# Optimization experiments

Hardware: AMD Instinct MI355X
Metric: run time of the kernel (lower is better)

The kernel has to match this reference:

```python
import jax, jax.numpy as jnp
import numpy as np

B, D_IN, T, H, OUT = 128, 128, 1024, 512, 2


def setup_inputs() -> dict:
    key = jax.random.key(0)
    ks = jax.random.split(key, 12)
    s = 1.0 / np.sqrt(H)  # torch LSTM/Linear init scale
    u = lambda k, shape: jax.random.uniform(k, shape, jnp.float32, -s, s)
    return {
        "x": jax.random.normal(ks[0], (B, D_IN, T), jnp.float32),
        # layer 0 (input_dim -> H), gate order i,f,g,o stacked along 4H
        "Wih0": u(ks[1], (4 * H, D_IN)),
        "Whh0": u(ks[2], (4 * H, H)),
        "bih0": u(ks[3], (4 * H,)),
        "bhh0": u(ks[4], (4 * H,)),
        # layer 1 (H -> H)
        "Wih1": u(ks[5], (4 * H, H)),
        "Whh1": u(ks[6], (4 * H, H)),
        "bih1": u(ks[7], (4 * H,)),
        "bhh1": u(ks[8], (4 * H,)),
        # linear head
        "fcW": u(ks[9], (OUT, H)),
        "fcb": u(ks[10], (OUT,)),
    }


def _lstm_layer(x_btd, Wih, Whh, bih, bhh):
    """One unidirectional LSTM layer. x_btd: (B,T,D). Returns (hs_bth, h_last)."""
    h_dim = Whh.shape[1]
    b = x_btd.shape[0]
    # precompute input contribution for all timesteps: (T, B, 4H)
    xg = jnp.einsum("btd,gd->tbg", x_btd, Wih) + (bih + bhh)

    def step(carry, xg_t):
        h, c = carry
        gates = xg_t + h @ Whh.T  # (B, 4H)
        i, f, g, o = jnp.split(gates, 4, axis=-1)
        i = jax.nn.sigmoid(i)
        f = jax.nn.sigmoid(f)
        g = jnp.tanh(g)
        o = jax.nn.sigmoid(o)
        c = f * c + i * g
        h = o * jnp.tanh(c)
        return (h, c), h

    h0 = jnp.zeros((b, h_dim), x_btd.dtype)
    c0 = jnp.zeros((b, h_dim), x_btd.dtype)
    (h_last, _), hs = jax.lax.scan(step, (h0, c0), xg)
    return jnp.transpose(hs, (1, 0, 2)), h_last  # (B,T,H), (B,H)


def reference(x, Wih0, Whh0, bih0, bhh0, Wih1, Whh1, bih1, bhh1, fcW, fcb):
    x_btd = jnp.transpose(x, (0, 2, 1))  # (B, T, D_IN), mirrors x.transpose(1,2)
    hs0, _ = _lstm_layer(x_btd, Wih0, Whh0, bih0, bhh0)
    _, h_last = _lstm_layer(hs0, Wih1, Whh1, bih1, bhh1)
    return h_last @ fcW.T + fcb  # fc(hidden[-1]) -> (B, OUT)
```

## Files before the change

kernel.cpp:

```cpp
#include <hip/hip_runtime.h>
#include <hip/hip_fp16.h>


typedef _Float16 half8 __attribute__((ext_vector_type(8)));
typedef float f32x4 __attribute__((ext_vector_type(4)));
typedef unsigned long long u64;
typedef u64 u64x2 __attribute__((ext_vector_type(2)));

#define MFMA16(a, b, c) __builtin_amdgcn_mfma_f32_16x16x32_f16((a), (b), (c), 0, 0, 0)

#define WS_H0_OFF (64 << 10)
#define WS_H1_OFF (576 << 10)
#define WS_XTW_OFF (832 << 10)
#define SYNC_CLAIM 1024
#define SYNC_MODE 1040
#define SYNC_ARRIVE 1056
#define SYNC_FLAG0 1280
#define SYNC_FLAG1 2304

__device__ __forceinline__ float sigf(float x) {
  return __builtin_amdgcn_rcpf(1.f + exp2f(-1.44269504f * x));
}
__device__ __forceinline__ float tanhf_(float x) {
  return 1.f - 2.f * __builtin_amdgcn_rcpf(1.f + exp2f(2.88539008f * x));
}
__device__ __forceinline__ unsigned short f2h(float x) {
  _Float16 h = (_Float16)x;
  unsigned short b;
  __builtin_memcpy(&b, &h, 2);
  return b;
}
__device__ __forceinline__ u64 lda(const u64* p) {
  return __hip_atomic_load(p, __ATOMIC_RELAXED, __HIP_MEMORY_SCOPE_AGENT);
}

__device__ __forceinline__ void cvt_split(const f32x4& a, const f32x4& b,
                                          half8& hi, half8& lo) {
#pragma unroll
  for (int i = 0; i < 4; ++i) {
    float w0 = a[i], w1 = b[i];
    _Float16 h0 = (_Float16)w0, h1 = (_Float16)w1;
    hi[i] = h0;
    hi[i + 4] = h1;
    lo[i] = (_Float16)((w0 - (float)h0) * 2048.0f);
    lo[i + 4] = (_Float16)((w1 - (float)h1) * 2048.0f);
  }
}
__device__ __forceinline__ half8 hscale(half8 v) {
  half8 r;
#pragma unroll
  for (int i = 0; i < 8; ++i) r[i] = v[i] * (_Float16)4.8828125e-4f;
  return r;
}

__global__ void __launch_bounds__(256) prep_kernel(const float* __restrict__ x,
                                                   _Float16* __restrict__ xTw,
                                                   unsigned* __restrict__ sync,
                                                   float* __restrict__ out) {
  const int bid = blockIdx.x;
  const int c = bid >> 4, b16 = bid & 15;
  const int tid = threadIdx.x;
  if (bid == 0) {
#pragma unroll
    for (int i = 0; i < 16; ++i) sync[i * 256 + tid] = 0;
    out[tid] = 0.f;
  }
  const int d = tid & 127, th = tid >> 7;
  const float* src = x + ((size_t)(c * 16 + b16) * 128 + d) * 1024 + th * 16;
  _Float16* dst = xTw + ((size_t)c * 32 + th * 16) * (16 * 128) + b16 * 128 + d;
#pragma unroll
  for (int i = 0; i < 16; ++i) dst[(size_t)i * (16 * 128)] = (_Float16)src[i];
}

__global__ void __launch_bounds__(256, 2) lstm_scan(
    const float* __restrict__ Whh0, const float* __restrict__ bih0,
    const float* __restrict__ bhh0, const float* __restrict__ Wih1,
    const float* __restrict__ Whh1, const float* __restrict__ bih1,
    const float* __restrict__ bhh1, const float* __restrict__ fcW,
    const float* __restrict__ fcb, const float* __restrict__ Wih0,
    const float* __restrict__ x, unsigned* __restrict__ sync,
    unsigned short* __restrict__ exch, _Float16* __restrict__ xTw,
    float* __restrict__ out) {
  __shared__ __align__(16) _Float16 hbuf[2][16][4][16][8];
  __shared__ unsigned s_bcast[2];

  const int tid = threadIdx.x;
  const int wave = tid >> 6;
  const int lane = tid & 63;
  const int q = lane >> 4;
  const int bb = lane & 15;

  unsigned xcc;
  asm("s_getreg_b32 %0, hwreg(HW_REG_XCC_ID)" : "=s"(xcc));
  xcc &= 7;
  unsigned* claim = sync + SYNC_CLAIM;
  unsigned* modew = sync + SYNC_MODE;
  unsigned* arrive = sync + SYNC_ARRIVE;
  if (tid == 0) {
    unsigned idx = __hip_atomic_fetch_add(claim + xcc, 1u, __ATOMIC_RELAXED,
                                          __HIP_MEMORY_SCOPE_AGENT);
    unsigned ord = __hip_atomic_fetch_add(arrive, 1u + (idx >> 31),
                                          __ATOMIC_RELAXED,
                                          __HIP_MEMORY_SCOPE_AGENT);
    if (ord == 511u) {
      unsigned ok = 1;
#pragma unroll
      for (int i = 0; i < 8; ++i)
        ok &= (__hip_atomic_load(claim + i, __ATOMIC_RELAXED,
                                 __HIP_MEMORY_SCOPE_AGENT) == 64u);
      __hip_atomic_store(modew, ok ? 2u : 1u, __ATOMIC_RELAXED,
                         __HIP_MEMORY_SCOPE_AGENT);
    }
    unsigned mv = 0;
    int guard = 0;
    for (;;) {
      mv = __hip_atomic_load(modew, __ATOMIC_RELAXED, __HIP_MEMORY_SCOPE_AGENT);
      if (mv != 0u) break;
      if (++guard > (1 << 18)) { mv = 1u; break; }
    }
    s_bcast[0] = mv;
    s_bcast[1] = idx;
  }
  __syncthreads();
  const bool loc = (s_bcast[0] == 2u);
  const unsigned idx = s_bcast[1];
  bool roleL1;
  int c, wg;
  if (loc) {
    c = (int)xcc;
    roleL1 = idx >= 32u;
    wg = roleL1 ? (int)idx - 32 : (int)idx;
  } else {
    const int b = blockIdx.x;
    roleL1 = b >= 256;
    const int b2 = roleL1 ? b - 256 : b;
    c = b2 >> 5;
    wg = b2 & 31;
  }

  const int wcl = wg * 4 + wave;
  const int chbase = wcl * 4;
  const int m = lane & 15;
  const int arow = (m & 3) * 512 + chbase + (m >> 2);
  unsigned short* xtw16 = (unsigned short*)xTw;
  unsigned short* exch1 = exch + ((512 << 10) >> 1);
  const int ch = chbase + q;
  const int hoff = (((ch >> 5) * 4 + ((ch >> 3) & 3)) * 16) * 8 + (ch & 7) +
                   bb * 8;

  unsigned* flag0 = sync + SYNC_FLAG0 + c * 128;
  unsigned* flag1 = sync + SYNC_FLAG1 + c * 128;
  const u64* s0p = (const u64*)flag0 + lane;
  const u64* s1p = (const u64*)flag1 + lane;
  const int T = 1024;

  if (!roleL1) {
    half8 fW0[16], fW0lo[16], fX[4], fXlo[4];
    {
      const float* p0 = Whh0 + (size_t)arow * 512 + q * 8;
#pragma unroll
      for (int kt = 0; kt < 16; ++kt) {
        f32x4 a0 = *(const f32x4*)(p0 + kt * 32),
              b0 = *(const f32x4*)(p0 + kt * 32 + 4);
        cvt_split(a0, b0, fW0[kt], fW0lo[kt]);
      }
      const float* p3 = Wih0 + (size_t)arow * 128 + q * 8;
#pragma unroll
      for (int kt = 0; kt < 4; ++kt) {
        f32x4 a3 = *(const f32x4*)(p3 + kt * 32),
              b3 = *(const f32x4*)(p3 + kt * 32 + 4);
        cvt_split(a3, b3, fX[kt], fXlo[kt]);
      }
    }
    float b0v[4];
#pragma unroll
    for (int g = 0; g < 4; ++g) {
      int rrow = g * 512 + chbase + q;
      b0v[g] = bih0[rrow] + bhh0[rrow];
    }

    float c0 = 0.f;
    for (int r = 0; r < T; ++r) {
      const bool doref = (wave == 2 && r < 992 && (r & 3) == 0);

      f32x4 xv4;
      int sw = 0, rw = 0, xb = 0, xd = 0;
      if (doref) {
        const int wnext = (r >> 5) + 1;
        sw = wnext % 3; rw = r & 31;
        xb = wg >> 1; xd = (wg & 1) * 64 + lane;
        xv4 = *(const f32x4*)(x + ((size_t)(c * 16 + xb) * 128 + xd) * 1024 +
                              wnext * 32 + rw);
      }

      half8 xf[4];
      {
        const int s = (r >> 5) % 3, tau = r & 31;
        const u64* xp = (const u64*)xtw16 +
                        (((size_t)(s * 8 + c) * 32 + tau) * 16 + bb) * 32;
        if (loc) {
#pragma unroll
          for (int kt = 0; kt < 4; ++kt)
            xf[kt] =
                __builtin_bit_cast(half8, *(const u64x2*)(xp + kt * 8 + q * 2));
        } else {
#pragma unroll
          for (int kt = 0; kt < 4; ++kt) {
            u64x2 t2;
            t2.x = lda(xp + kt * 8 + q * 2);
            t2.y = lda(xp + kt * 8 + q * 2 + 1);
            xf[kt] = __builtin_bit_cast(half8, t2);
          }
        }
      }

      if (r > 0) {
        int guard = 0;
        for (;;) {
          u64 f0 = lda(s0p), f1 = lda(s1p);
          bool ok = ((int)(unsigned)f0 >= r) && ((int)(f0 >> 32) >= r) &&
                    ((int)(unsigned)f1 >= r - 3) && ((int)(f1 >> 32) >= r - 3);
          if (__ballot(ok) == ~0ull) break;
          if (++guard > 4096) break;
        }
        asm volatile("" ::: "memory");
        if (loc) {
          const u64x2* src =
              (const u64x2*)exch + ((size_t)((r - 1) & 3) * 8 + c) * 1024 + tid;
          u64x2 v[4];
#pragma unroll
          for (int i = 0; i < 4; ++i) v[i] = src[i * 256];
          u64x2* dst = (u64x2*)hbuf + tid;
#pragma unroll
          for (int i = 0; i < 4; ++i) dst[i * 256] = v[i];
        } else {
          const u64* src =
              (const u64*)exch + ((size_t)((r - 1) & 3) * 8 + c) * 2048 + tid;
          u64 v[8];
#pragma unroll
          for (int i = 0; i < 8; ++i) v[i] = lda(src + i * 256);
          u64* dst = (u64*)hbuf + tid;
#pragma unroll
          for (int i = 0; i < 8; ++i) dst[i * 256] = v[i];
        }
      }
      __syncthreads();

      f32x4 accX = {b0v[0], b0v[1], b0v[2], b0v[3]};
#pragma unroll
      for (int kt = 0; kt < 4; ++kt) {
        accX = MFMA16(fX[kt], xf[kt], accX);
        accX = MFMA16(fXlo[kt], hscale(xf[kt]), accX);
      }
      f32x4 a0 = {0.f, 0.f, 0.f, 0.f};
      f32x4 a0b = a0, a0l = a0, a0bl = a0;
      if (r > 0) {
#pragma unroll
        for (int kt = 0; kt < 8; ++kt) {
          half8 hA = *(const half8*)(&hbuf[0][kt][q][bb][0]);
          half8 hB = *(const half8*)(&hbuf[0][kt + 8][q][bb][0]);
          a0 = MFMA16(fW0[kt], hA, a0);
          a0b = MFMA16(fW0[kt + 8], hB, a0b);
          a0l = MFMA16(fW0lo[kt], hscale(hA), a0l);
          a0bl = MFMA16(fW0lo[kt + 8], hscale(hB), a0bl);
        }
      }
      f32x4 g0 = accX + ((a0 + a0b) + (a0l + a0bl));
      float gi = sigf(g0.x), gf = sigf(g0.y), gg = tanhf_(g0.z),
            go = sigf(g0.w);
      c0 = gf * c0 + gi * gg;
      float h0v = go * tanhf_(c0);
      size_t hidx = ((size_t)(r & 3) * 8 + c) * 8192 + hoff;
      if (loc)
        exch[hidx] = f2h(h0v);
      else
        __hip_atomic_store(exch + hidx, f2h(h0v), __ATOMIC_RELAXED,
                           __HIP_MEMORY_SCOPE_AGENT);

      if (doref) {
#pragma unroll
        for (int j = 0; j < 4; ++j) {
          size_t xidx =
              (((size_t)(sw * 8 + c) * 32 + rw + j) * 16 + xb) * 128 + xd;
          if (loc)
            xtw16[xidx] = f2h(xv4[j]);
          else
            __hip_atomic_store(xtw16 + xidx, f2h(xv4[j]), __ATOMIC_RELAXED,
                               __HIP_MEMORY_SCOPE_AGENT);
        }
      }

      asm volatile("s_waitcnt vmcnt(0)" ::: "memory");
      if (lane == 0) {
        if (loc)
          __hip_atomic_store(flag0 + wcl, (unsigned)(r + 1), __ATOMIC_RELAXED,
                             __HIP_MEMORY_SCOPE_WORKGROUP);
        else
          __hip_atomic_store(flag0 + wcl, (unsigned)(r + 1), __ATOMIC_RELAXED,
                             __HIP_MEMORY_SCOPE_AGENT);
      }
    }
  } else {
    half8 fW1i[16], fW1ilo[16], fW1h[16];
    {
      const float* p1 = Wih1 + (size_t)arow * 512 + q * 8;
      const float* p2 = Whh1 + (size_t)arow * 512 + q * 8;
#pragma unroll
      for (int kt = 0; kt < 16; ++kt) {
        f32x4 a1 = *(const f32x4*)(p1 + kt * 32),
              b1 = *(const f32x4*)(p1 + kt * 32 + 4);
        cvt_split(a1, b1, fW1i[kt], fW1ilo[kt]);
        f32x4 a2 = *(const f32x4*)(p2 + kt * 32),
              b2 = *(const f32x4*)(p2 + kt * 32 + 4);
        half8 dummy;
        cvt_split(a2, b2, fW1h[kt], dummy);
      }
    }
    float b1v[4];
#pragma unroll
    for (int g = 0; g < 4; ++g) {
      int rrow = g * 512 + chbase + q;
      b1v[g] = bih1[rrow] + bhh1[rrow];
    }
    const float fcw0 = fcW[ch], fcw1 = fcW[512 + ch];

    float c1 = 0.f;
    for (int t = 0; t < T; ++t) {
      {
        int guard = 0;
        for (;;) {
          u64 f0 = lda(s0p), f1 = lda(s1p);
          bool ok = ((int)(unsigned)f0 >= t + 1) && ((int)(f0 >> 32) >= t + 1) &&
                    ((int)(unsigned)f1 >= t) && ((int)(f1 >> 32) >= t);
          if (__ballot(ok) == ~0ull) break;
          if (++guard > 4096) break;
        }
        asm volatile("" ::: "memory");
      }
      if (loc) {
        const u64x2* src0 =
            (const u64x2*)exch + ((size_t)(t & 3) * 8 + c) * 1024 + tid;
        u64x2 v0[4];
#pragma unroll
        for (int i = 0; i < 4; ++i) v0[i] = src0[i * 256];
        u64x2* dst0 = (u64x2*)hbuf + tid;
#pragma unroll
        for (int i = 0; i < 4; ++i) dst0[i * 256] = v0[i];
        if (t > 0) {
          const u64x2* src1 = (const u64x2*)exch1 +
                              ((size_t)((t - 1) & 1) * 8 + c) * 1024 + tid;
          u64x2 v1[4];
#pragma unroll
          for (int i = 0; i < 4; ++i) v1[i] = src1[i * 256];
          u64x2* dst1 = (u64x2*)hbuf + 1024 + tid;
#pragma unroll
          for (int i = 0; i < 4; ++i) dst1[i * 256] = v1[i];
        }
      } else {
        const u64* src0 =
            (const u64*)exch + ((size_t)(t & 3) * 8 + c) * 2048 + tid;
        u64 v0[8];
#pragma unroll
        for (int i = 0; i < 8; ++i) v0[i] = lda(src0 + i * 256);
        u64* dst0 = (u64*)hbuf + tid;
#pragma unroll
        for (int i = 0; i < 8; ++i) dst0[i * 256] = v0[i];
        if (t > 0) {
          const u64* src1 =
              (const u64*)exch1 + ((size_t)((t - 1) & 1) * 8 + c) * 2048 + tid;
          u64 v1[8];
#pragma unroll
          for (int i = 0; i < 8; ++i) v1[i] = lda(src1 + i * 256);
          u64* dst1 = (u64*)hbuf + 2048 + tid;
#pragma unroll
          for (int i = 0; i < 8; ++i) dst1[i * 256] = v1[i];
        }
      }
      __syncthreads();

      f32x4 a1 = {b1v[0], b1v[1], b1v[2], b1v[3]};
      f32x4 a1b = {0.f, 0.f, 0.f, 0.f};
      f32x4 a1c = a1b, a1d = a1b;
#pragma unroll
      for (int kt = 0; kt < 8; ++kt) {
        half8 hA = *(const half8*)(&hbuf[0][kt][q][bb][0]);
        half8 hB = *(const half8*)(&hbuf[0][kt + 8][q][bb][0]);
        a1 = MFMA16(fW1i[kt], hA, a1);
        a1b = MFMA16(fW1i[kt + 8], hB, a1b);
        a1 = MFMA16(fW1ilo[kt], hscale(hA), a1);
        a1b = MFMA16(fW1ilo[kt + 8], hscale(hB), a1b);
      }
      if (t > 0) {
#pragma unroll
        for (int kt = 0; kt < 8; ++kt) {
          half8 hC = *(const half8*)(&hbuf[1][kt][q][bb][0]);
          half8 hD = *(const half8*)(&hbuf[1][kt + 8][q][bb][0]);
          a1c = MFMA16(fW1h[kt], hC, a1c);
          a1d = MFMA16(fW1h[kt + 8], hD, a1d);
        }
      }
      f32x4 g1 = (a1 + a1b) + (a1c + a1d);
      float gi = sigf(g1.x), gf = sigf(g1.y), gg = tanhf_(g1.z),
            go = sigf(g1.w);
      c1 = gf * c1 + gi * gg;
      float h1v = go * tanhf_(c1);

      if (t == T - 1) {
        float s0 = h1v * fcw0, s1 = h1v * fcw1;
        s0 += __shfl_xor(s0, 16); s0 += __shfl_xor(s0, 32);
        s1 += __shfl_xor(s1, 16); s1 += __shfl_xor(s1, 32);
        if (q == 0) {
          atomicAdd(out + (size_t)(c * 16 + bb) * 2 + 0, s0);
          atomicAdd(out + (size_t)(c * 16 + bb) * 2 + 1, s1);
        }
        if (wcl == 0 && lane < 32)
          atomicAdd(out + (size_t)(c * 16 + (lane & 15)) * 2 + (lane >> 4),
                    fcb[lane >> 4]);
      } else {
        size_t hidx = ((size_t)(t & 1) * 8 + c) * 8192 + hoff;
        if (loc)
          exch1[hidx] = f2h(h1v);
        else
          __hip_atomic_store(exch1 + hidx, f2h(h1v), __ATOMIC_RELAXED,
                             __HIP_MEMORY_SCOPE_AGENT);
      }
      asm volatile("s_waitcnt vmcnt(0)" ::: "memory");
      if (lane == 0) {
        if (loc)
          __hip_atomic_store(flag1 + wcl, (unsigned)(t + 1), __ATOMIC_RELAXED,
                             __HIP_MEMORY_SCOPE_WORKGROUP);
        else
          __hip_atomic_store(flag1 + wcl, (unsigned)(t + 1), __ATOMIC_RELAXED,
                             __HIP_MEMORY_SCOPE_AGENT);
      }
    }
  }
}

extern "C" void kernel_launch(void* const* d_in, const int* in_sizes, int n_in,
                              void* d_out, int out_size, void* d_ws,
                              size_t ws_size, hipStream_t stream) {
  const float* x = (const float*)d_in[0];
  const float* Wih0 = (const float*)d_in[1];
  const float* Whh0 = (const float*)d_in[2];
  const float* bih0 = (const float*)d_in[3];
  const float* bhh0 = (const float*)d_in[4];
  const float* Wih1 = (const float*)d_in[5];
  const float* Whh1 = (const float*)d_in[6];
  const float* bih1 = (const float*)d_in[7];
  const float* bhh1 = (const float*)d_in[8];
  const float* fcW = (const float*)d_in[9];
  const float* fcb = (const float*)d_in[10];

  char* ws = (char*)d_ws;
  unsigned* sync = (unsigned*)ws;
  unsigned short* exch = (unsigned short*)(ws + WS_H0_OFF);
  _Float16* xTw = (_Float16*)(ws + WS_XTW_OFF);
  float* out = (float*)d_out;

  prep_kernel<<<dim3(128), dim3(256), 0, stream>>>(x, xTw, sync, out);
  lstm_scan<<<dim3(512), dim3(256), 0, stream>>>(Whh0, bih0, bhh0, Wih1, Whh1,
                                                 bih1, bhh1, fcW, fcb, Wih0, x,
                                                 sync, exch, xTw, out);
}
```

Baseline: 3.040 ms.

## Shorten LSTM recurrence critical path by hoisting input-gate MFMAs off the wait

Layer-0 blocks now compute the x-projection MFMAs before spinning on the neighbour flags, and publish their h0 readiness flag before the x-transpose writes. Layer-1 blocks split the input-from-h0 contribution out of the dependent step and compute it for step t+1 right after publishing h1 for step t. This leaves only the Whh1 recurrent product on the layer-1 critical path. A third LDS buffer holds the prefetched h0 tiles. The cost is extra LDS, additional __syncthreads, and a more complex flag protocol that risks ordering or staleness bugs.

```diff
diff --git a/kernel.cpp b/kernel.cpp
--- a/kernel.cpp
+++ b/kernel.cpp
@@ -81,7 +81,7 @@
     const float* __restrict__ x, unsigned* __restrict__ sync,
     unsigned short* __restrict__ exch, _Float16* __restrict__ xTw,
     float* __restrict__ out) {
-  __shared__ __align__(16) _Float16 hbuf[2][16][4][16][8];
+  __shared__ __align__(16) _Float16 hbuf[3][16][4][16][8];
   __shared__ unsigned s_bcast[2];
 
   const int tid = threadIdx.x;
@@ -214,6 +214,13 @@
         }
       }
 
+      f32x4 accX = {b0v[0], b0v[1], b0v[2], b0v[3]};
+#pragma unroll
+      for (int kt = 0; kt < 4; ++kt) {
+        accX = MFMA16(fX[kt], xf[kt], accX);
+        accX = MFMA16(fXlo[kt], hscale(xf[kt]), accX);
+      }
+
       if (r > 0) {
         int guard = 0;
         for (;;) {
@@ -230,7 +237,7 @@
           u64x2 v[4];
 #pragma unroll
           for (int i = 0; i < 4; ++i) v[i] = src[i * 256];
-          u64x2* dst = (u64x2*)hbuf + tid;
+          u64x2* dst = (u64x2*)hbuf[0] + tid;
 #pragma unroll
           for (int i = 0; i < 4; ++i) dst[i * 256] = v[i];
         } else {
@@ -239,19 +246,13 @@
           u64 v[8];
 #pragma unroll
           for (int i = 0; i < 8; ++i) v[i] = lda(src + i * 256);
-          u64* dst = (u64*)hbuf + tid;
+          u64* dst = (u64*)hbuf[0] + tid;
 #pragma unroll
           for (int i = 0; i < 8; ++i) dst[i * 256] = v[i];
         }
       }
       __syncthreads();
 
-      f32x4 accX = {b0v[0], b0v[1], b0v[2], b0v[3]};
-#pragma unroll
-      for (int kt = 0; kt < 4; ++kt) {
-        accX = MFMA16(fX[kt], xf[kt], accX);
-        accX = MFMA16(fXlo[kt], hscale(xf[kt]), accX);
-      }
       f32x4 a0 = {0.f, 0.f, 0.f, 0.f};
       f32x4 a0b = a0, a0l = a0, a0bl = a0;
       if (r > 0) {
@@ -277,6 +278,16 @@
         __hip_atomic_store(exch + hidx, f2h(h0v), __ATOMIC_RELAXED,
                            __HIP_MEMORY_SCOPE_AGENT);
 
+      asm volatile("s_waitcnt vmcnt(0)" ::: "memory");
+      if (lane == 0) {
+        if (loc)
+          __hip_atomic_store(flag0 + wcl, (unsigned)(r + 1), __ATOMIC_RELAXED,
+                             __HIP_MEMORY_SCOPE_WORKGROUP);
+        else
+          __hip_atomic_store(flag0 + wcl, (unsigned)(r + 1), __ATOMIC_RELAXED,
+                             __HIP_MEMORY_SCOPE_AGENT);
+      }
+
       if (doref) {
 #pragma unroll
         for (int j = 0; j < 4; ++j) {
@@ -289,16 +300,6 @@
                                __HIP_MEMORY_SCOPE_AGENT);
         }
       }
-
-      asm volatile("s_waitcnt vmcnt(0)" ::: "memory");
-      if (lane == 0) {
-        if (loc)
-          __hip_atomic_store(flag0 + wcl, (unsigned)(r + 1), __ATOMIC_RELAXED,
-                             __HIP_MEMORY_SCOPE_WORKGROUP);
-        else
-          __hip_atomic_store(flag0 + wcl, (unsigned)(r + 1), __ATOMIC_RELAXED,
-                             __HIP_MEMORY_SCOPE_AGENT);
-      }
     }
   } else {
     half8 fW1i[16], fW1ilo[16], fW1h[16];
@@ -325,76 +326,86 @@
     const float fcw0 = fcW[ch], fcw1 = fcW[512 + ch];
 
     float c1 = 0.f;
-    for (int t = 0; t < T; ++t) {
-      {
-        int guard = 0;
-        for (;;) {
-          u64 f0 = lda(s0p), f1 = lda(s1p);
-          bool ok = ((int)(unsigned)f0 >= t + 1) && ((int)(f0 >> 32) >= t + 1) &&
-                    ((int)(unsigned)f1 >= t) && ((int)(f1 >> 32) >= t);
-          if (__ballot(ok) == ~0ull) break;
-          if (++guard > 4096) break;
-        }
-        asm volatile("" ::: "memory");
-      }
+    f32x4 a1 = {b1v[0], b1v[1], b1v[2], b1v[3]};
+    f32x4 a1b = {0.f, 0.f, 0.f, 0.f};
+
+    {
+      int guard = 0;
+      for (;;) {
+        u64 f0 = lda(s0p);
+        bool ok = ((int)(unsigned)f0 >= 1) && ((int)(f0 >> 32) >= 1);
+        if (__ballot(ok) == ~0ull) break;
+        if (++guard > 8192) break;
+      }
+      asm volatile("" ::: "memory");
       if (loc) {
-        const u64x2* src0 =
-            (const u64x2*)exch + ((size_t)(t & 3) * 8 + c) * 1024 + tid;
-        u64x2 v0[4];
-#pragma unroll
-        for (int i = 0; i < 4; ++i) v0[i] = src0[i * 256];
-        u64x2* dst0 = (u64x2*)hbuf + tid;
-#pragma unroll
-        for (int i = 0; i < 4; ++i) dst0[i * 256] = v0[i];
-        if (t > 0) {
-          const u64x2* src1 = (const u64x2*)exch1 +
-                              ((size_t)((t - 1) & 1) * 8 + c) * 1024 + tid;
-          u64x2 v1[4];
-#pragma unroll
-          for (int i = 0; i < 4; ++i) v1[i] = src1[i * 256];
-          u64x2* dst1 = (u64x2*)hbuf + 1024 + tid;
-#pragma unroll
-          for (int i = 0; i < 4; ++i) dst1[i * 256] = v1[i];
-        }
+        const u64x2* src = (const u64x2*)exch + (size_t)c * 1024 + tid;
+        u64x2 v[4];
+#pragma unroll
+        for (int i = 0; i < 4; ++i) v[i] = src[i * 256];
+        u64x2* dst = (u64x2*)hbuf[1] + tid;
+#pragma unroll
+        for (int i = 0; i < 4; ++i) dst[i * 256] = v[i];
       } else {
-        const u64* src0 =
-            (const u64*)exch + ((size_t)(t & 3) * 8 + c) * 2048 + tid;
-        u64 v0[8];
-#pragma unroll
-        for (int i = 0; i < 8; ++i) v0[i] = lda(src0 + i * 256);
-        u64* dst0 = (u64*)hbuf + tid;
-#pragma unroll
-        for (int i = 0; i < 8; ++i) dst0[i * 256] = v0[i];
-        if (t > 0) {
-          const u64* src1 =
-              (const u64*)exch1 + ((size_t)((t - 1) & 1) * 8 + c) * 2048 + tid;
-          u64 v1[8];
-#pragma unroll
-          for (int i = 0; i < 8; ++i) v1[i] = lda(src1 + i * 256);
-          u64* dst1 = (u64*)hbuf + 2048 + tid;
-#pragma unroll
-          for (int i = 0; i < 8; ++i) dst1[i * 256] = v1[i];
-        }
+        const u64* src = (const u64*)exch + (size_t)c * 2048 + tid;
+        u64 v[8];
+#pragma unroll
+        for (int i = 0; i < 8; ++i) v[i] = lda(src + i * 256);
+        u64* dst = (u64*)hbuf[1] + tid;
+#pragma unroll
+        for (int i = 0; i < 8; ++i) dst[i * 256] = v[i];
       }
       __syncthreads();
-
-      f32x4 a1 = {b1v[0], b1v[1], b1v[2], b1v[3]};
-      f32x4 a1b = {0.f, 0.f, 0.f, 0.f};
-      f32x4 a1c = a1b, a1d = a1b;
 #pragma unroll
       for (int kt = 0; kt < 8; ++kt) {
-        half8 hA = *(const half8*)(&hbuf[0][kt][q][bb][0]);
-        half8 hB = *(const half8*)(&hbuf[0][kt + 8][q][bb][0]);
+        half8 hA = *(const half8*)(&hbuf[1][kt][q][bb][0]);
+        half8 hB = *(const half8*)(&hbuf[1][kt + 8][q][bb][0]);
         a1 = MFMA16(fW1i[kt], hA, a1);
         a1b = MFMA16(fW1i[kt + 8], hB, a1b);
         a1 = MFMA16(fW1ilo[kt], hscale(hA), a1);
         a1b = MFMA16(fW1ilo[kt + 8], hscale(hB), a1b);
       }
+    }
+
+    for (int t = 0; t < T; ++t) {
       if (t > 0) {
+        int guard = 0;
+        for (;;) {
+          u64 f1 = lda(s1p);
+          bool ok = ((int)(unsigned)f1 >= t) && ((int)(f1 >> 32) >= t);
+          if (__ballot(ok) == ~0ull) break;
+          if (++guard > 4096) break;
+        }
+        asm volatile("" ::: "memory");
+        if (loc) {
+          const u64x2* src = (const u64x2*)exch1 +
+                             ((size_t)((t - 1) & 1) * 8 + c) * 1024 + tid;
+          u64x2 v[4];
+#pragma unroll
+          for (int i = 0; i < 4; ++i) v[i] = src[i * 256];
+          u64x2* dst = (u64x2*)hbuf[0] + tid;
+#pragma unroll
+          for (int i = 0; i < 4; ++i) dst[i * 256] = v[i];
+        } else {
+          const u64* src =
+              (const u64*)exch1 + ((size_t)((t - 1) & 1) * 8 + c) * 2048 + tid;
+          u64 v[8];
+#pragma unroll
+          for (int i = 0; i < 8; ++i) v[i] = lda(src + i * 256);
+          u64* dst = (u64*)hbuf[0] + tid;
+#pragma unroll
+          for (int i = 0; i < 8; ++i) dst[i * 256] = v[i];
+        }
+      }
+      __syncthreads();
+
+      f32x4 a1c = {0.f, 0.f, 0.f, 0.f};
+      f32x4 a1d = a1c;
+      if (t > 0) {
 #pragma unroll
         for (int kt = 0; kt < 8; ++kt) {
-          half8 hC = *(const half8*)(&hbuf[1][kt][q][bb][0]);
-          half8 hD = *(const half8*)(&hbuf[1][kt + 8][q][bb][0]);
+          half8 hC = *(const half8*)(&hbuf[0][kt][q][bb][0]);
+          half8 hD = *(const half8*)(&hbuf[0][kt + 8][q][bb][0]);
           a1c = MFMA16(fW1h[kt], hC, a1c);
           a1d = MFMA16(fW1h[kt + 8], hD, a1d);
         }
@@ -432,6 +443,49 @@
         else
           __hip_atomic_store(flag1 + wcl, (unsigned)(t + 1), __ATOMIC_RELAXED,
                              __HIP_MEMORY_SCOPE_AGENT);
+      }
+
+      if (t < T - 1) {
+        int guard = 0;
+        for (;;) {
+          u64 f0 = lda(s0p);
+          bool ok = ((int)(unsigned)f0 >= t + 2) && ((int)(f0 >> 32) >= t + 2);
+          if (__ballot(ok) == ~0ull) break;
+          if (++guard > 4096) break;
+        }
+        asm volatile("" ::: "memory");
+        const int buf = 1 + ((t + 1) & 1);
+        if (loc) {
+          const u64x2* src = (const u64x2*)exch +
+                             ((size_t)((t + 1) & 3) * 8 + c) * 1024 + tid;
+          u64x2 v[4];
+#pragma unroll
+          for (int i = 0; i < 4; ++i) v[i] = src[i * 256];
+          u64x2* dst = (u64x2*)hbuf[buf] + tid;
+#pragma unroll
+          for (int i = 0; i < 4; ++i) dst[i * 256] = v[i];
+        } else {
+          const u64* src =
+              (const u64*)exch + ((size_t)((t + 1) & 3) * 8 + c) * 2048 + tid;
+          u64 v[8];
+#pragma unroll
+          for (int i = 0; i < 8; ++i) v[i] = lda(src + i * 256);
+          u64* dst = (u64*)hbuf[buf] + tid;
+#pragma unroll
+          for (int i = 0; i < 8; ++i) dst[i * 256] = v[i];
+        }
+        __syncthreads();
+        a1 = {b1v[0], b1v[1], b1v[2], b1v[3]};
+        a1b = {0.f, 0.f, 0.f, 0.f};
+#pragma unroll
+        for (int kt = 0; kt < 8; ++kt) {
+          half8 hA = *(const half8*)(&hbuf[buf][kt][q][bb][0]);
+          half8 hB = *(const half8*)(&hbuf[buf][kt + 8][q][bb][0]);
+          a1 = MFMA16(fW1i[kt], hA, a1);
+          a1b = MFMA16(fW1i[kt + 8], hB, a1b);
+          a1 = MFMA16(fW1ilo[kt], hscale(hA), a1);
+          a1b = MFMA16(fW1ilo[kt + 8], hscale(hB), a1b);
+        }
       }
     }
   }
```

After: 2.888 ms. 5.0% less time.
